# Kernel tuning notes

Hardware: AMD Instinct MI355X
Metric: run time of the kernel (lower is better)

The kernel has to match this reference:

```python
import jax, jax.numpy as jnp
import numpy as np

B, N_RELS, DICT, FEAT, LAT = 2048, 512, 2000, 300, 512
TOPK, DISK, T = 3, 20, 0.07


def setup_inputs() -> dict:
    key = jax.random.key(0)
    ks = jax.random.split(key, 24)
    p = lambda i, s: jax.random.normal(ks[i], s, jnp.float32) * 0.05
    return {
        "logits": jax.random.normal(ks[0], (B, N_RELS), jnp.float32),
        "rels": jax.random.randint(ks[1], (N_RELS, 2), 0, DICT, jnp.int32),
        "rel_dict": jax.random.uniform(ks[2], (DICT, FEAT), jnp.float32),
        "fc1_w": p(3, (2 * FEAT, 300)), "fc1_b": p(4, (300,)),
        "fc2mu_w": p(5, (300, LAT)), "fc2mu_b": p(6, (LAT,)),
        "fc2ls_w": p(7, (300, LAT)), "fc2ls_b": p(8, (LAT,)),
        "fc3_w": p(9, (LAT + FEAT, 300)), "fc3_b": p(10, (300,)),
        "fc4_w": p(11, (300, FEAT)), "fc4_b": p(12, (FEAT,)),
        "qi1_w": p(13, (FEAT, 512)), "qi1_b": p(14, (512,)),
        "qi2_w": p(15, (512, 512)), "qi2_b": p(16, (512,)),
        "qz1_w": p(17, (LAT, 512)), "qz1_b": p(18, (512,)),
        "qz2_w": p(19, (512, 512)), "qz2_b": p(20, (512,)),
        "eps1": jax.random.normal(ks[21], (B, LAT), jnp.float32),
        "eps2": jax.random.normal(ks[22], (B, LAT), jnp.float32),
    }


def _enc2(v, w1, b1, w2, b2):
    # two-layer MLP with LeakyReLU(0.2), matches nn.Sequential in MoCo
    h = jax.nn.leaky_relu(v @ w1 + b1, 0.2)
    return jax.nn.leaky_relu(h @ w2 + b2, 0.2)


def reference(logits, rels, rel_dict, fc1_w, fc1_b, fc2mu_w, fc2mu_b,
              fc2ls_w, fc2ls_b, fc3_w, fc3_b, fc4_w, fc4_b,
              qi1_w, qi1_b, qi2_w, qi2_b, qz1_w, qz1_b, qz2_w, qz2_b,
              eps1, eps2):
    # top-3 (descending sort head) and bottom-20 (ascending sort head)
    _, top_idx = jax.lax.top_k(logits, TOPK)            # [B,3]
    _, dis_idx = jax.lax.top_k(-logits, DISK)           # [B,20]
    pos = rel_dict[rels[top_idx, 1]]                    # [B,3,FEAT]
    pos1 = pos[:, 0]                                    # [B,FEAT] condition / MoCo positive
    x = pos[:, 0] * pos[:, 1] * pos[:, 2]               # elementwise product of top-3 dict vecs
    neg = rel_dict[rels[dis_idx, 1]]                    # [B,20,FEAT]

    # CVAE encode / reparametrize / decode (batched over the python loop)
    h1 = jax.nn.relu(jnp.concatenate([x, pos1], axis=-1) @ fc1_w + fc1_b)
    mu = h1 @ fc2mu_w + fc2mu_b                          # [B,512]
    log_std = h1 @ fc2ls_w + fc2ls_b                     # [B,512]
    std = jnp.exp(log_std)
    z = mu + eps1 * std
    h3 = jax.nn.relu(jnp.concatenate([z, pos1], axis=-1) @ fc3_w + fc3_b)
    recon = jax.nn.sigmoid(h3 @ fc4_w + fc4_b)           # [B,FEAT]
    recon_loss = jnp.sum((recon - x) ** 2)
    kl = jnp.sum(-0.5 * (1.0 + 2.0 * log_std - mu ** 2 - jnp.exp(2.0 * log_std)))
    loss_vae = (recon_loss + kl).reshape(1)

    # second reparametrize draw feeds MoCo
    z_ = mu + eps2 * std

    # MoCo: encoder_k == encoder_inp (copied at init; momentum update preserves equality)
    z_p = _enc2(z_, qz1_w, qz1_b, qz2_w, qz2_b)          # [B,512]
    pos_vec = _enc2(pos1, qi1_w, qi1_b, qi2_w, qi2_b)    # [B,512]
    neg_p = jax.lax.stop_gradient(_enc2(neg, qi1_w, qi1_b, qi2_w, qi2_b))  # [B,20,512]
    pos_l = jnp.sum(z_p * pos_vec, axis=-1, keepdims=True)                 # [B,1]
    neg_l = jnp.einsum('bd,bnd->bn', z_p, neg_p)                           # [B,20]
    lg = jnp.concatenate([pos_l, neg_l], axis=-1) / T                      # [B,21]
    # per-sample CE with label 0 (batch=1 in original loop), summed across loop
    loss_csl = jnp.sum(-jax.nn.log_softmax(lg, axis=-1)[:, 0]).reshape(1)

    z_rel = jnp.concatenate([jnp.zeros((1, z_p.shape[1]), z_p.dtype), z_p], axis=0)  # [B+1,512]
    return loss_vae, loss_csl, z_rel
```

## Files before the change

kernel.cpp:

```cpp
#include <hip/hip_runtime.h>
#include <math.h>

#define B      2048
#define NRELS  512
#define FEAT   300
#define LAT    512

typedef __attribute__((ext_vector_type(8))) short short8;
typedef __attribute__((ext_vector_type(4))) float f32x4;

__device__ inline short f2bf(float f) {
    union { float f; unsigned u; } v; v.f = f;
    unsigned u = v.u;
    u += 0x7fffu + ((u >> 16) & 1u);
    return (short)(u >> 16);
}

struct WDesc { const float* src; short* dst; int K, N, Kpad, Npad, ilv, ilvoff; };
struct WPack { WDesc d[9]; };

__global__ __launch_bounds__(256) void stage0(WPack p,
                                              const float* __restrict__ logits,
                                              const int* __restrict__ rels,
                                              const float* __restrict__ rel_dict,
                                              int* __restrict__ top_idx,
                                              int* __restrict__ dis_idx,
                                              short* __restrict__ xcat,
                                              float* __restrict__ xf,
                                              short* __restrict__ zcat,
                                              short* __restrict__ Rb,
                                              float* __restrict__ acc,
                                              float* __restrict__ out)
{
    const int bid = blockIdx.x;
    if (bid < 512) {
        if (bid == 0 && threadIdx.x >= 252) ((unsigned*)acc)[threadIdx.x - 252] = 0u;
        int lane = threadIdx.x & 63;
        int row  = bid * 4 + (threadIdx.x >> 6);
        const float* pl = logits + (size_t)row * NRELS;
        float v[8];
#pragma unroll
        for (int j = 0; j < 8; ++j) v[j] = pl[j * 64 + lane];
        float w[8];
#pragma unroll
        for (int j = 0; j < 8; ++j) w[j] = v[j];
        for (int t = 0; t < 20; ++t) {
            float bv = __builtin_inff(); int bi = 0x7fffffff;
#pragma unroll
            for (int j = 0; j < 8; ++j) {
                int idx = j * 64 + lane;
                if (w[j] < bv || (w[j] == bv && idx < bi)) { bv = w[j]; bi = idx; }
            }
#pragma unroll
            for (int off = 32; off >= 1; off >>= 1) {
                float ov = __shfl_xor(bv, off);
                int   oi = __shfl_xor(bi, off);
                if (ov < bv || (ov == bv && oi < bi)) { bv = ov; bi = oi; }
            }
            if ((bi & 63) == lane) w[bi >> 6] = __builtin_inff();
            if (lane == 0) dis_idx[row * 20 + t] = bi;
        }
        int t3[3];
#pragma unroll
        for (int j = 0; j < 8; ++j) w[j] = v[j];
        for (int t = 0; t < 3; ++t) {
            float bv = -__builtin_inff(); int bi = 0x7fffffff;
#pragma unroll
            for (int j = 0; j < 8; ++j) {
                int idx = j * 64 + lane;
                if (w[j] > bv || (w[j] == bv && idx < bi)) { bv = w[j]; bi = idx; }
            }
#pragma unroll
            for (int off = 32; off >= 1; off >>= 1) {
                float ov = __shfl_xor(bv, off);
                int   oi = __shfl_xor(bi, off);
                if (ov > bv || (ov == bv && oi < bi)) { bv = ov; bi = oi; }
            }
            if ((bi & 63) == lane) w[bi >> 6] = -__builtin_inff();
            t3[t] = bi;
        }
        if (lane == 0) top_idx[row] = t3[0];
        int i0 = rels[2 * t3[0] + 1];
        int i1 = rels[2 * t3[1] + 1];
        int i2 = rels[2 * t3[2] + 1];
        const float* r0 = rel_dict + (size_t)i0 * FEAT;
        const float* r1 = rel_dict + (size_t)i1 * FEAT;
        const float* r2 = rel_dict + (size_t)i2 * FEAT;
        short* xd  = xcat + (size_t)row * 640;
        short* zd  = zcat + (size_t)row * 832;
        float* xfd = xf   + (size_t)row * 300;
        for (int c = lane; c < FEAT; c += 64) {
            float a = r0[c];
            float x = a * r1[c] * r2[c];
            xd[c]       = f2bf(x);
            xd[300 + c] = f2bf(a);
            zd[512 + c] = f2bf(a);
            xfd[c]      = x;
        }
        if (lane < 40) xd[600 + lane] = 0;
        if (lane < 20) zd[812 + lane] = 0;
    } else if (bid < 640) {
        int lane = threadIdx.x & 63;
        int j = (bid - 512) * 4 + (threadIdx.x >> 6);
        int id = rels[2 * j + 1];
        const float* src = rel_dict + (size_t)id * FEAT;
        for (int c = lane; c < 320; c += 64)
            Rb[(size_t)j * 320 + c] = (c < FEAT) ? f2bf(src[c]) : (short)0;
    } else if (bid < 928) {
        int rel = bid - 640;
        WDesc w = p.d[rel >> 5];
        int b32 = rel & 31;
        if (!w.ilv) {
            int total = w.Npad * w.Kpad;
            for (int i = b32 * 256 + threadIdx.x; i < total; i += 32 * 256) {
                int n = i / w.Kpad, k = i - n * w.Kpad;
                w.dst[i] = (n < w.N && k < w.K) ? f2bf(w.src[(size_t)k * w.N + n]) : (short)0;
            }
        } else {
            int total = w.N * w.Kpad;
            for (int i = b32 * 256 + threadIdx.x; i < total; i += 32 * 256) {
                int c = i / w.Kpad, k = i - c * w.Kpad;
                int n = ((c >> 5) << 6) + w.ilvoff + (c & 31);
                w.dst[(size_t)n * w.Kpad + k] = (k < w.K) ? f2bf(w.src[(size_t)k * w.N + c]) : (short)0;
            }
        }
    } else {
        out[2 + threadIdx.x]       = 0.f;
        out[2 + 256 + threadIdx.x] = 0.f;
    }
}

template<int ACT, int MODE>
__device__ __attribute__((always_inline)) void gemm_core(
    short (&As)[64][72], short (&Bs)[64][72],
    int bx, int by,
    const short* __restrict__ A, const short* __restrict__ Bt,
    const float* __restrict__ bias, const float* __restrict__ bias2,
    void* __restrict__ Cv, int Nreal, int Kpad, int ldc,
    const float* __restrict__ aux0, const float* __restrict__ aux1,
    short* __restrict__ z0, short* __restrict__ z1,
    float* __restrict__ accv)
{
    const int wave = threadIdx.x >> 6;
    const int lane = threadIdx.x & 63;
    const int row0 = by * 64;
    const int col0 = bx * 64;

    const int srow = threadIdx.x >> 3;
    const int sk   = (threadIdx.x & 7) * 8;
    const short* Ap0 = A  + (size_t)(row0 + srow)      * Kpad + sk;
    const short* Ap1 = A  + (size_t)(row0 + srow + 32) * Kpad + sk;
    const short* Bp0 = Bt + (size_t)(col0 + srow)      * Kpad + sk;
    const short* Bp1 = Bt + (size_t)(col0 + srow + 32) * Kpad + sk;

    const int frow = lane & 15;
    const int fk   = (lane >> 4) * 8;

    f32x4 acc0 = {0,0,0,0}, acc1 = {0,0,0,0}, acc2 = {0,0,0,0}, acc3 = {0,0,0,0};

    short8 a0 = *(const short8*)Ap0;
    short8 a1 = *(const short8*)Ap1;
    short8 b0 = *(const short8*)Bp0;
    short8 b1 = *(const short8*)Bp1;

    for (int k0 = 0; k0 < Kpad; k0 += 64) {
        *(short8*)&As[srow][sk]      = a0;
        *(short8*)&As[srow + 32][sk] = a1;
        *(short8*)&Bs[srow][sk]      = b0;
        *(short8*)&Bs[srow + 32][sk] = b1;
        __syncthreads();
        int kn = k0 + 64;
        if (kn < Kpad) {
            a0 = *(const short8*)(Ap0 + kn);
            a1 = *(const short8*)(Ap1 + kn);
            b0 = *(const short8*)(Bp0 + kn);
            b1 = *(const short8*)(Bp1 + kn);
        }
        short8 af0 = *(const short8*)&As[wave * 16 + frow][fk];
        short8 af1 = *(const short8*)&As[wave * 16 + frow][fk + 32];
        short8 bf00 = *(const short8*)&Bs[ 0 + frow][fk];
        short8 bf01 = *(const short8*)&Bs[ 0 + frow][fk + 32];
        short8 bf10 = *(const short8*)&Bs[16 + frow][fk];
        short8 bf11 = *(const short8*)&Bs[16 + frow][fk + 32];
        short8 bf20 = *(const short8*)&Bs[32 + frow][fk];
        short8 bf21 = *(const short8*)&Bs[32 + frow][fk + 32];
        short8 bf30 = *(const short8*)&Bs[48 + frow][fk];
        short8 bf31 = *(const short8*)&Bs[48 + frow][fk + 32];
        acc0 = __builtin_amdgcn_mfma_f32_16x16x32_bf16(af0, bf00, acc0, 0, 0, 0);
        acc1 = __builtin_amdgcn_mfma_f32_16x16x32_bf16(af0, bf10, acc1, 0, 0, 0);
        acc2 = __builtin_amdgcn_mfma_f32_16x16x32_bf16(af0, bf20, acc2, 0, 0, 0);
        acc3 = __builtin_amdgcn_mfma_f32_16x16x32_bf16(af0, bf30, acc3, 0, 0, 0);
        acc0 = __builtin_amdgcn_mfma_f32_16x16x32_bf16(af1, bf01, acc0, 0, 0, 0);
        acc1 = __builtin_amdgcn_mfma_f32_16x16x32_bf16(af1, bf11, acc1, 0, 0, 0);
        acc2 = __builtin_amdgcn_mfma_f32_16x16x32_bf16(af1, bf21, acc2, 0, 0, 0);
        acc3 = __builtin_amdgcn_mfma_f32_16x16x32_bf16(af1, bf31, acc3, 0, 0, 0);
        __syncthreads();
    }

    const int orow = row0 + wave * 16 + (lane >> 4) * 4;
    f32x4 accs[4] = {acc0, acc1, acc2, acc3};

    if (MODE == 3) {
        float kls = 0.f;
#pragma unroll
        for (int n0 = 0; n0 < 2; ++n0) {
            int zc = bx * 32 + n0 * 16 + frow;
            float bmu = bias[zc];
            float bls = bias2[zc];
#pragma unroll
            for (int j = 0; j < 4; ++j) {
                int row = orow + j;
                float m = accs[n0][j]     + bmu;
                float l = accs[n0 + 2][j] + bls;
                float s = expf(l);
                size_t ei = (size_t)row * 512 + zc;
                z0[(size_t)row * 832 + zc] = f2bf(m + aux0[ei] * s);
                z1[ei]                     = f2bf(m + aux1[ei] * s);
                kls += -0.5f * (1.f + 2.f * l - m * m - expf(2.f * l));
            }
        }
#pragma unroll
        for (int off = 32; off >= 1; off >>= 1) kls += __shfl_xor(kls, off);
        __shared__ float redS[4];
        if (lane == 0) redS[wave] = kls;
        __syncthreads();
        if (threadIdx.x == 0) atomicAdd(accv, redS[0] + redS[1] + redS[2] + redS[3]);
        return;
    }

    float fsum = 0.f;
#pragma unroll
    for (int n0 = 0; n0 < 4; ++n0) {
        int col = col0 + n0 * 16 + frow;
        float bs = bias[col < Nreal ? col : Nreal - 1];
#pragma unroll
        for (int j = 0; j < 4; ++j) {
            float v = accs[n0][j] + bs;
            if (ACT == 1)      v = v > 0.f ? v : 0.f;
            else if (ACT == 2) v = v > 0.f ? v : 0.2f * v;
            else if (ACT == 3) v = 1.f / (1.f + expf(-v));
            if (MODE == 2) {
                if (col < Nreal) {
                    float d = v - aux0[(size_t)(orow + j) * 300 + col];
                    fsum += d * d;
                }
            } else {
                size_t idx = (size_t)(orow + j) * ldc + col;
                if (MODE == 1) ((float*)Cv)[idx] = v;
                else           ((short*)Cv)[idx] = f2bf(v);
            }
        }
    }
    if (MODE == 2) {
#pragma unroll
        for (int off = 32; off >= 1; off >>= 1) fsum += __shfl_xor(fsum, off);
        __shared__ float redF[4];
        if (lane == 0) redF[wave] = fsum;
        __syncthreads();
        if (threadIdx.x == 0) atomicAdd(accv, redF[0] + redF[1] + redF[2] + redF[3]);
    }
}

__global__ __launch_bounds__(256) void stage1(const short* Rb, const short* w_qi1t, const float* qi1_b, short* Ehb,
                                              const short* xcat, const short* w_fc1t, const float* fc1_b, short* h1)
{
    __shared__ short As[64][72];
    __shared__ short Bs[64][72];
    int b = blockIdx.x;
    if (b < 64)
        gemm_core<2,0>(As, Bs, b & 7, b >> 3, Rb, w_qi1t, qi1_b, qi1_b, Ehb, 512, 320, 512,
                       nullptr, nullptr, nullptr, nullptr, nullptr);
    else {
        b -= 64;
        gemm_core<1,0>(As, Bs, b % 5, b / 5, xcat, w_fc1t, fc1_b, fc1_b, h1, 300, 640, 320,
                       nullptr, nullptr, nullptr, nullptr, nullptr);
    }
}

__global__ __launch_bounds__(256) void stage2(const short* Ehb, const short* w_qi2t, const float* qi2_b, float* E,
                                              const short* h1, const short* w_mulst,
                                              const float* mu_b, const float* ls_b,
                                              const float* eps1, const float* eps2,
                                              short* zcat, short* zb, float* acc)
{
    __shared__ short As[64][72];
    __shared__ short Bs[64][72];
    int b = blockIdx.x;
    if (b < 64)
        gemm_core<2,1>(As, Bs, b & 7, b >> 3, Ehb, w_qi2t, qi2_b, qi2_b, E, 512, 512, 512,
                       nullptr, nullptr, nullptr, nullptr, nullptr);
    else {
        b -= 64;
        gemm_core<0,3>(As, Bs, b & 15, b >> 4, h1, w_mulst, mu_b, ls_b, nullptr, 1024, 320, 0,
                       eps1, eps2, zcat, zb, acc);
    }
}

__global__ __launch_bounds__(256) void stage3(const short* zcat, const short* w_fc3t, const float* fc3_b, short* h3,
                                              const short* zb, const short* w_qz1t, const float* qz1_b, short* t1)
{
    __shared__ short As[64][72];
    __shared__ short Bs[64][72];
    int b = blockIdx.x;
    if (b < 160)
        gemm_core<1,0>(As, Bs, b % 5, b / 5, zcat, w_fc3t, fc3_b, fc3_b, h3, 300, 832, 320,
                       nullptr, nullptr, nullptr, nullptr, nullptr);
    else {
        b -= 160;
        gemm_core<2,0>(As, Bs, b & 7, b >> 3, zb, w_qz1t, qz1_b, qz1_b, t1, 512, 512, 512,
                       nullptr, nullptr, nullptr, nullptr, nullptr);
    }
}

__global__ __launch_bounds__(256) void stage4(const short* h3, const short* w_fc4t, const float* fc4_b,
                                              const float* xf, float* acc,
                                              const short* t1, const short* w_qz2t, const float* qz2_b, float* zp)
{
    __shared__ short As[64][72];
    __shared__ short Bs[64][72];
    int b = blockIdx.x;
    if (b < 160)
        gemm_core<3,2>(As, Bs, b % 5, b / 5, h3, w_fc4t, fc4_b, fc4_b, nullptr, 300, 320, 0,
                       xf, nullptr, nullptr, nullptr, acc + 1);
    else {
        b -= 160;
        gemm_core<2,1>(As, Bs, b & 7, b >> 3, t1, w_qz2t, qz2_b, qz2_b, zp, 512, 512, 512,
                       nullptr, nullptr, nullptr, nullptr, nullptr);
    }
}

__global__ __launch_bounds__(256) void stage5(const float* __restrict__ zp,
                                              const float* __restrict__ E,
                                              const int* __restrict__ top_idx,
                                              const int* __restrict__ dis_idx,
                                              float* __restrict__ acc,
                                              float* __restrict__ out)
{
    int lane = threadIdx.x & 63;
    int wave = threadIdx.x >> 6;
    int r    = blockIdx.x * 4 + wave;
    const float* z = zp + (size_t)r * LAT;
    const float4 za = reinterpret_cast<const float4*>(z)[lane * 2 + 0];
    const float4 zb = reinterpret_cast<const float4*>(z)[lane * 2 + 1];

    int ids[21];
    ids[0] = top_idx[r];
#pragma unroll
    for (int n = 0; n < 20; ++n) ids[n + 1] = dis_idx[r * 20 + n];

    float lg[21];
#pragma unroll
    for (int t = 0; t < 21; ++t) {
        const float* e = E + (size_t)ids[t] * LAT;
        const float4 ea = reinterpret_cast<const float4*>(e)[lane * 2 + 0];
        const float4 eb = reinterpret_cast<const float4*>(e)[lane * 2 + 1];
        float d = za.x * ea.x + za.y * ea.y + za.z * ea.z + za.w * ea.w
                + zb.x * eb.x + zb.y * eb.y + zb.z * eb.z + zb.w * eb.w;
#pragma unroll
        for (int off = 32; off >= 1; off >>= 1) d += __shfl_xor(d, off);
        lg[t] = d / 0.07f;
    }
    float m = lg[0];
#pragma unroll
    for (int t = 1; t < 21; ++t) m = fmaxf(m, lg[t]);
    float s = 0.f;
#pragma unroll
    for (int t = 0; t < 21; ++t) s += expf(lg[t] - m);
    float loss = logf(s) + m - lg[0];

    __shared__ float red[4];
    if (lane == 0) red[wave] = loss;
    __syncthreads();
    if (threadIdx.x == 0) {
        atomicAdd(&acc[2], red[0] + red[1] + red[2] + red[3]);
        __threadfence();
        unsigned old = atomicAdd((unsigned*)acc + 3, 1u);
        if (old == (unsigned)(gridDim.x - 1)) {
            __threadfence();
            volatile float* va = acc;
            out[0] = va[0] + va[1];
            out[1] = va[2];
        }
    }
}

extern "C" void kernel_launch(void* const* d_in, const int* in_sizes, int n_in,
                              void* d_out, int out_size, void* d_ws, size_t ws_size,
                              hipStream_t stream)
{
    const float* logits   = (const float*)d_in[0];
    const int*   rels     = (const int*)  d_in[1];
    const float* rel_dict = (const float*)d_in[2];
    const float* fc1_w    = (const float*)d_in[3];
    const float* fc1_b    = (const float*)d_in[4];
    const float* fc2mu_w  = (const float*)d_in[5];
    const float* fc2mu_b  = (const float*)d_in[6];
    const float* fc2ls_w  = (const float*)d_in[7];
    const float* fc2ls_b  = (const float*)d_in[8];
    const float* fc3_w    = (const float*)d_in[9];
    const float* fc3_b    = (const float*)d_in[10];
    const float* fc4_w    = (const float*)d_in[11];
    const float* fc4_b    = (const float*)d_in[12];
    const float* qi1_w    = (const float*)d_in[13];
    const float* qi1_b    = (const float*)d_in[14];
    const float* qi2_w    = (const float*)d_in[15];
    const float* qi2_b    = (const float*)d_in[16];
    const float* qz1_w    = (const float*)d_in[17];
    const float* qz1_b    = (const float*)d_in[18];
    const float* qz2_w    = (const float*)d_in[19];
    const float* qz2_b    = (const float*)d_in[20];
    const float* eps1     = (const float*)d_in[21];
    const float* eps2     = (const float*)d_in[22];
    float* out = (float*)d_out;

    char* wsb = (char*)d_ws;
    size_t off = 0;
    auto alloc = [&](size_t bytes) -> void* {
        off = (off + 255) & ~(size_t)255;
        void* p = wsb + off;
        off += bytes;
        return p;
    };
    float* acc     = (float*)alloc(16);
    int*   top_idx = (int*)  alloc((size_t)B * 4);
    int*   dis_idx = (int*)  alloc((size_t)B * 20 * 4);
    short* Rb      = (short*)alloc((size_t)NRELS * 320 * 2);
    short* Ehb     = (short*)alloc((size_t)NRELS * 512 * 2);
    float* E       = (float*)alloc((size_t)NRELS * 512 * 4);
    short* xcat    = (short*)alloc((size_t)B * 640 * 2);
    float* xf      = (float*)alloc((size_t)B * 300 * 4);
    short* h1      = (short*)alloc((size_t)B * 320 * 2);
    short* zcat    = (short*)alloc((size_t)B * 832 * 2);
    short* zb      = (short*)alloc((size_t)B * 512 * 2);
    short* h3      = (short*)alloc((size_t)B * 320 * 2);
    short* t1      = (short*)alloc((size_t)B * 512 * 2);

    short* w_qi1t  = (short*)alloc((size_t)512 * 320 * 2);
    short* w_qi2t  = (short*)alloc((size_t)512 * 512 * 2);
    short* w_fc1t  = (short*)alloc((size_t)320 * 640 * 2);
    short* w_mulst = (short*)alloc((size_t)1024 * 320 * 2);
    short* w_fc3t  = (short*)alloc((size_t)320 * 832 * 2);
    short* w_fc4t  = (short*)alloc((size_t)320 * 320 * 2);
    short* w_qz1t  = (short*)alloc((size_t)512 * 512 * 2);
    short* w_qz2t  = (short*)alloc((size_t)512 * 512 * 2);

    WPack p;
    p.d[0] = {qi1_w,   w_qi1t,  300, 512, 320,  512, 0, 0};
    p.d[1] = {qi2_w,   w_qi2t,  512, 512, 512,  512, 0, 0};
    p.d[2] = {fc1_w,   w_fc1t,  600, 300, 640,  320, 0, 0};
    p.d[3] = {fc2mu_w, w_mulst, 300, 512, 320, 1024, 1, 0};
    p.d[4] = {fc2ls_w, w_mulst, 300, 512, 320, 1024, 1, 32};
    p.d[5] = {fc3_w,   w_fc3t,  812, 300, 832,  320, 0, 0};
    p.d[6] = {fc4_w,   w_fc4t,  300, 300, 320,  320, 0, 0};
    p.d[7] = {qz1_w,   w_qz1t,  512, 512, 512,  512, 0, 0};
    p.d[8] = {qz2_w,   w_qz2t,  512, 512, 512,  512, 0, 0};

    float* zp = out + 2 + 512;

    stage0<<<929, 256, 0, stream>>>(p, logits, rels, rel_dict, top_idx, dis_idx,
                                    xcat, xf, zcat, Rb, acc, out);
    stage1<<<224, 256, 0, stream>>>(Rb, w_qi1t, qi1_b, Ehb, xcat, w_fc1t, fc1_b, h1);
    stage2<<<576, 256, 0, stream>>>(Ehb, w_qi2t, qi2_b, E, h1, w_mulst, fc2mu_b, fc2ls_b,
                                    eps1, eps2, zcat, zb, acc);
    stage3<<<416, 256, 0, stream>>>(zcat, w_fc3t, fc3_b, h3, zb, w_qz1t, qz1_b, t1);
    stage4<<<416, 256, 0, stream>>>(h3, w_fc4t, fc4_b, xf, acc, t1, w_qz2t, qz2_b, zp);
    stage5<<<B / 4, 256, 0, stream>>>(zp, E, top_idx, dis_idx, acc, out);
}
```

Before: 97.75 us.

## Use 128x64 GEMM tiles for batch GEMMs and tile-transpose weight conversion

Adds a gemm_tile path where each wave computes a 32x64 sub-tile, so each block covers 128 rows instead of 64 for the batch-sized GEMMs. This halves block counts and doubles reuse of the B tile per LDS load. The weight transpose-to-bf16 pass now stages 64x64 tiles through shared memory, giving coalesced reads and writes instead of strided global reads. The cost is fewer blocks per stage, which lowers occupancy and parallelism on a large GPU, plus a larger LDS footprint.

```diff
diff --git a/kernel.cpp b/kernel.cpp
--- a/kernel.cpp
+++ b/kernel.cpp
@@ -16,7 +16,7 @@
     return (short)(u >> 16);
 }
 
-struct WDesc { const float* src; short* dst; int K, N, Kpad, Npad, ilv, ilvoff; };
+struct WDesc { const float* src; short* dst; int K, N, Kpad, Npad, ilv, ilvoff, tstart, tk; };
 struct WPack { WDesc d[9]; };
 
 __global__ __launch_bounds__(256) void stage0(WPack p,
@@ -32,6 +32,7 @@
                                               float* __restrict__ acc,
                                               float* __restrict__ out)
 {
+    __shared__ float T[64][65];
     const int bid = blockIdx.x;
     if (bid < 512) {
         if (bid == 0 && threadIdx.x >= 252) ((unsigned*)acc)[threadIdx.x - 252] = 0u;
@@ -106,22 +107,40 @@
         const float* src = rel_dict + (size_t)id * FEAT;
         for (int c = lane; c < 320; c += 64)
             Rb[(size_t)j * 320 + c] = (c < FEAT) ? f2bf(src[c]) : (short)0;
-    } else if (bid < 928) {
-        int rel = bid - 640;
-        WDesc w = p.d[rel >> 5];
-        int b32 = rel & 31;
-        if (!w.ilv) {
-            int total = w.Npad * w.Kpad;
-            for (int i = b32 * 256 + threadIdx.x; i < total; i += 32 * 256) {
-                int n = i / w.Kpad, k = i - n * w.Kpad;
-                w.dst[i] = (n < w.N && k < w.K) ? f2bf(w.src[(size_t)k * w.N + n]) : (short)0;
-            }
-        } else {
-            int total = w.N * w.Kpad;
-            for (int i = b32 * 256 + threadIdx.x; i < total; i += 32 * 256) {
-                int c = i / w.Kpad, k = i - c * w.Kpad;
-                int n = ((c >> 5) << 6) + w.ilvoff + (c & 31);
-                w.dst[(size_t)n * w.Kpad + k] = (k < w.K) ? f2bf(w.src[(size_t)k * w.N + c]) : (short)0;
+    } else if (bid < 1092) {
+        int u = bid - 640;
+        int di = 0;
+#pragma unroll
+        for (int q = 1; q < 9; ++q) if (u >= p.d[q].tstart) di = q;
+        WDesc w = p.d[di];
+        int r  = u - w.tstart;
+        int kt = r % w.tk;
+        int nt = r / w.tk;
+        int k0 = kt * 64, n0 = nt * 64;
+
+        {
+            int kk = threadIdx.x >> 2;
+            int c0 = (threadIdx.x & 3) * 16;
+            int gk = k0 + kk;
+            const float* srow = w.src + (size_t)gk * w.N;
+            bool kin = gk < w.K;
+#pragma unroll
+            for (int j = 0; j < 16; ++j) {
+                int gn = n0 + c0 + j;
+                T[kk][c0 + j] = (kin && gn < w.N) ? srow[gn] : 0.f;
+            }
+        }
+        __syncthreads();
+        {
+            int nn = threadIdx.x >> 2;
+            int c0 = (threadIdx.x & 3) * 16;
+            int ns = n0 + nn;
+            if (ns < w.Npad || w.ilv) {
+                int nd = w.ilv ? (((ns >> 5) << 6) + w.ilvoff + (ns & 31)) : ns;
+                short* drow = w.dst + (size_t)nd * w.Kpad + k0;
+#pragma unroll
+                for (int j = 0; j < 16; ++j)
+                    drow[c0 + j] = f2bf(T[c0 + j][nn]);
             }
         }
     } else {
@@ -132,8 +151,85 @@
 
 template<int ACT, int MODE>
 __device__ __attribute__((always_inline)) void gemm_core(
-    short (&As)[64][72], short (&Bs)[64][72],
+    short (&As)[128][72], short (&Bs)[64][72],
     int bx, int by,
+    const short* __restrict__ A, const short* __restrict__ Bt,
+    const float* __restrict__ bias,
+    void* __restrict__ Cv, int Nreal, int Kpad, int ldc)
+{
+    const int wave = threadIdx.x >> 6;
+    const int lane = threadIdx.x & 63;
+    const int row0 = by * 64;
+    const int col0 = bx * 64;
+
+    const int srow = threadIdx.x >> 3;
+    const int sk   = (threadIdx.x & 7) * 8;
+    const short* Ap0 = A  + (size_t)(row0 + srow)      * Kpad + sk;
+    const short* Ap1 = A  + (size_t)(row0 + srow + 32) * Kpad + sk;
+    const short* Bp0 = Bt + (size_t)(col0 + srow)      * Kpad + sk;
+    const short* Bp1 = Bt + (size_t)(col0 + srow + 32) * Kpad + sk;
+
+    const int frow = lane & 15;
+    const int fk   = (lane >> 4) * 8;
+
+    f32x4 acc0 = {0,0,0,0}, acc1 = {0,0,0,0}, acc2 = {0,0,0,0}, acc3 = {0,0,0,0};
+
+    short8 a0 = *(const short8*)Ap0;
+    short8 a1 = *(const short8*)Ap1;
+    short8 b0 = *(const short8*)Bp0;
+    short8 b1 = *(const short8*)Bp1;
+
+    for (int k0 = 0; k0 < Kpad; k0 += 64) {
+        *(short8*)&As[srow][sk]      = a0;
+        *(short8*)&As[srow + 32][sk] = a1;
+        *(short8*)&Bs[srow][sk]      = b0;
+        *(short8*)&Bs[srow + 32][sk] = b1;
+        __syncthreads();
+        int kn = k0 + 64;
+        if (kn < Kpad) {
+            a0 = *(const short8*)(Ap0 + kn);
+            a1 = *(const short8*)(Ap1 + kn);
+            b0 = *(const short8*)(Bp0 + kn);
+            b1 = *(const short8*)(Bp1 + kn);
+        }
+#pragma unroll
+        for (int kk = 0; kk < 2; ++kk) {
+            short8 af = *(const short8*)&As[wave * 16 + frow][fk + kk * 32];
+            short8 bf0 = *(const short8*)&Bs[ 0 + frow][fk + kk * 32];
+            short8 bf1 = *(const short8*)&Bs[16 + frow][fk + kk * 32];
+            short8 bf2 = *(const short8*)&Bs[32 + frow][fk + kk * 32];
+            short8 bf3 = *(const short8*)&Bs[48 + frow][fk + kk * 32];
+            acc0 = __builtin_amdgcn_mfma_f32_16x16x32_bf16(af, bf0, acc0, 0, 0, 0);
+            acc1 = __builtin_amdgcn_mfma_f32_16x16x32_bf16(af, bf1, acc1, 0, 0, 0);
+            acc2 = __builtin_amdgcn_mfma_f32_16x16x32_bf16(af, bf2, acc2, 0, 0, 0);
+            acc3 = __builtin_amdgcn_mfma_f32_16x16x32_bf16(af, bf3, acc3, 0, 0, 0);
+        }
+        __syncthreads();
+    }
+
+    const int orow = row0 + wave * 16 + (lane >> 4) * 4;
+    f32x4 accs[4] = {acc0, acc1, acc2, acc3};
+#pragma unroll
+    for (int n0 = 0; n0 < 4; ++n0) {
+        int col = col0 + n0 * 16 + frow;
+        float bs = bias[col < Nreal ? col : Nreal - 1];
+#pragma unroll
+        for (int j = 0; j < 4; ++j) {
+            float v = accs[n0][j] + bs;
+            if (ACT == 1)      v = v > 0.f ? v : 0.f;
+            else if (ACT == 2) v = v > 0.f ? v : 0.2f * v;
+            else if (ACT == 3) v = 1.f / (1.f + expf(-v));
+            size_t idx = (size_t)(orow + j) * ldc + col;
+            if (MODE == 1) ((float*)Cv)[idx] = v;
+            else           ((short*)Cv)[idx] = f2bf(v);
+        }
+    }
+}
+
+template<int ACT, int MODE>
+__device__ __attribute__((always_inline)) void gemm_tile(
+    short (&As)[128][72], short (&Bs)[64][72],
+    int tx, int ty,
     const short* __restrict__ A, const short* __restrict__ Bt,
     const float* __restrict__ bias, const float* __restrict__ bias2,
     void* __restrict__ Cv, int Nreal, int Kpad, int ldc,
@@ -141,88 +237,91 @@
     short* __restrict__ z0, short* __restrict__ z1,
     float* __restrict__ accv)
 {
-    const int wave = threadIdx.x >> 6;
+    const int w    = threadIdx.x >> 6;
     const int lane = threadIdx.x & 63;
-    const int row0 = by * 64;
-    const int col0 = bx * 64;
-
-    const int srow = threadIdx.x >> 3;
-    const int sk   = (threadIdx.x & 7) * 8;
-    const short* Ap0 = A  + (size_t)(row0 + srow)      * Kpad + sk;
-    const short* Ap1 = A  + (size_t)(row0 + srow + 32) * Kpad + sk;
-    const short* Bp0 = Bt + (size_t)(col0 + srow)      * Kpad + sk;
-    const short* Bp1 = Bt + (size_t)(col0 + srow + 32) * Kpad + sk;
-
+    const int row0 = ty * 128, col0 = tx * 64;
+
+    const int sr = threadIdx.x >> 3;
+    const int sk = (threadIdx.x & 7) * 8;
+    const short* Ap = A  + (size_t)(row0 + sr) * Kpad + sk;
+    const short* Bp = Bt + (size_t)(col0 + sr) * Kpad + sk;
     const int frow = lane & 15;
     const int fk   = (lane >> 4) * 8;
 
-    f32x4 acc0 = {0,0,0,0}, acc1 = {0,0,0,0}, acc2 = {0,0,0,0}, acc3 = {0,0,0,0};
-
-    short8 a0 = *(const short8*)Ap0;
-    short8 a1 = *(const short8*)Ap1;
-    short8 b0 = *(const short8*)Bp0;
-    short8 b1 = *(const short8*)Bp1;
+    f32x4 acc[2][4] = {};
+
+    short8 ra0 = *(const short8*)(Ap);
+    short8 ra1 = *(const short8*)(Ap + (size_t)32 * Kpad);
+    short8 ra2 = *(const short8*)(Ap + (size_t)64 * Kpad);
+    short8 ra3 = *(const short8*)(Ap + (size_t)96 * Kpad);
+    short8 rb0 = *(const short8*)(Bp);
+    short8 rb1 = *(const short8*)(Bp + (size_t)32 * Kpad);
 
     for (int k0 = 0; k0 < Kpad; k0 += 64) {
-        *(short8*)&As[srow][sk]      = a0;
-        *(short8*)&As[srow + 32][sk] = a1;
-        *(short8*)&Bs[srow][sk]      = b0;
-        *(short8*)&Bs[srow + 32][sk] = b1;
+        *(short8*)&As[sr     ][sk] = ra0;
+        *(short8*)&As[sr + 32][sk] = ra1;
+        *(short8*)&As[sr + 64][sk] = ra2;
+        *(short8*)&As[sr + 96][sk] = ra3;
+        *(short8*)&Bs[sr     ][sk] = rb0;
+        *(short8*)&Bs[sr + 32][sk] = rb1;
         __syncthreads();
         int kn = k0 + 64;
         if (kn < Kpad) {
-            a0 = *(const short8*)(Ap0 + kn);
-            a1 = *(const short8*)(Ap1 + kn);
-            b0 = *(const short8*)(Bp0 + kn);
-            b1 = *(const short8*)(Bp1 + kn);
-        }
-        short8 af0 = *(const short8*)&As[wave * 16 + frow][fk];
-        short8 af1 = *(const short8*)&As[wave * 16 + frow][fk + 32];
-        short8 bf00 = *(const short8*)&Bs[ 0 + frow][fk];
-        short8 bf01 = *(const short8*)&Bs[ 0 + frow][fk + 32];
-        short8 bf10 = *(const short8*)&Bs[16 + frow][fk];
-        short8 bf11 = *(const short8*)&Bs[16 + frow][fk + 32];
-        short8 bf20 = *(const short8*)&Bs[32 + frow][fk];
-        short8 bf21 = *(const short8*)&Bs[32 + frow][fk + 32];
-        short8 bf30 = *(const short8*)&Bs[48 + frow][fk];
-        short8 bf31 = *(const short8*)&Bs[48 + frow][fk + 32];
-        acc0 = __builtin_amdgcn_mfma_f32_16x16x32_bf16(af0, bf00, acc0, 0, 0, 0);
-        acc1 = __builtin_amdgcn_mfma_f32_16x16x32_bf16(af0, bf10, acc1, 0, 0, 0);
-        acc2 = __builtin_amdgcn_mfma_f32_16x16x32_bf16(af0, bf20, acc2, 0, 0, 0);
-        acc3 = __builtin_amdgcn_mfma_f32_16x16x32_bf16(af0, bf30, acc3, 0, 0, 0);
-        acc0 = __builtin_amdgcn_mfma_f32_16x16x32_bf16(af1, bf01, acc0, 0, 0, 0);
-        acc1 = __builtin_amdgcn_mfma_f32_16x16x32_bf16(af1, bf11, acc1, 0, 0, 0);
-        acc2 = __builtin_amdgcn_mfma_f32_16x16x32_bf16(af1, bf21, acc2, 0, 0, 0);
-        acc3 = __builtin_amdgcn_mfma_f32_16x16x32_bf16(af1, bf31, acc3, 0, 0, 0);
-        __syncthreads();
-    }
-
-    const int orow = row0 + wave * 16 + (lane >> 4) * 4;
-    f32x4 accs[4] = {acc0, acc1, acc2, acc3};
+            ra0 = *(const short8*)(Ap + kn);
+            ra1 = *(const short8*)(Ap + (size_t)32 * Kpad + kn);
+            ra2 = *(const short8*)(Ap + (size_t)64 * Kpad + kn);
+            ra3 = *(const short8*)(Ap + (size_t)96 * Kpad + kn);
+            rb0 = *(const short8*)(Bp + kn);
+            rb1 = *(const short8*)(Bp + (size_t)32 * Kpad + kn);
+        }
+#pragma unroll
+        for (int kk = 0; kk < 2; ++kk) {
+            short8 a0 = *(const short8*)&As[w * 32 +      frow][fk + kk * 32];
+            short8 a1 = *(const short8*)&As[w * 32 + 16 + frow][fk + kk * 32];
+            short8 b0 = *(const short8*)&Bs[ 0 + frow][fk + kk * 32];
+            short8 b1 = *(const short8*)&Bs[16 + frow][fk + kk * 32];
+            short8 b2 = *(const short8*)&Bs[32 + frow][fk + kk * 32];
+            short8 b3 = *(const short8*)&Bs[48 + frow][fk + kk * 32];
+            acc[0][0] = __builtin_amdgcn_mfma_f32_16x16x32_bf16(a0, b0, acc[0][0], 0, 0, 0);
+            acc[0][1] = __builtin_amdgcn_mfma_f32_16x16x32_bf16(a0, b1, acc[0][1], 0, 0, 0);
+            acc[0][2] = __builtin_amdgcn_mfma_f32_16x16x32_bf16(a0, b2, acc[0][2], 0, 0, 0);
+            acc[0][3] = __builtin_amdgcn_mfma_f32_16x16x32_bf16(a0, b3, acc[0][3], 0, 0, 0);
+            acc[1][0] = __builtin_amdgcn_mfma_f32_16x16x32_bf16(a1, b0, acc[1][0], 0, 0, 0);
+            acc[1][1] = __builtin_amdgcn_mfma_f32_16x16x32_bf16(a1, b1, acc[1][1], 0, 0, 0);
+            acc[1][2] = __builtin_amdgcn_mfma_f32_16x16x32_bf16(a1, b2, acc[1][2], 0, 0, 0);
+            acc[1][3] = __builtin_amdgcn_mfma_f32_16x16x32_bf16(a1, b3, acc[1][3], 0, 0, 0);
+        }
+        __syncthreads();
+    }
+
+    const int rbase = row0 + w * 32 + (lane >> 4) * 4;
 
     if (MODE == 3) {
         float kls = 0.f;
 #pragma unroll
-        for (int n0 = 0; n0 < 2; ++n0) {
-            int zc = bx * 32 + n0 * 16 + frow;
-            float bmu = bias[zc];
-            float bls = bias2[zc];
-#pragma unroll
-            for (int j = 0; j < 4; ++j) {
-                int row = orow + j;
-                float m = accs[n0][j]     + bmu;
-                float l = accs[n0 + 2][j] + bls;
-                float s = expf(l);
-                size_t ei = (size_t)row * 512 + zc;
-                z0[(size_t)row * 832 + zc] = f2bf(m + aux0[ei] * s);
-                z1[ei]                     = f2bf(m + aux1[ei] * s);
-                kls += -0.5f * (1.f + 2.f * l - m * m - expf(2.f * l));
+        for (int mr = 0; mr < 2; ++mr) {
+#pragma unroll
+            for (int nc = 0; nc < 2; ++nc) {
+                int zc = tx * 32 + nc * 16 + frow;
+                float bmu = bias[zc];
+                float bls = bias2[zc];
+#pragma unroll
+                for (int j = 0; j < 4; ++j) {
+                    int row = rbase + mr * 16 + j;
+                    float m = acc[mr][nc][j]     + bmu;
+                    float l = acc[mr][nc + 2][j] + bls;
+                    float s = expf(l);
+                    size_t ei = (size_t)row * 512 + zc;
+                    z0[(size_t)row * 832 + zc] = f2bf(m + aux0[ei] * s);
+                    z1[ei]                     = f2bf(m + aux1[ei] * s);
+                    kls += -0.5f * (1.f + 2.f * l - m * m - expf(2.f * l));
+                }
             }
         }
 #pragma unroll
         for (int off = 32; off >= 1; off >>= 1) kls += __shfl_xor(kls, off);
         __shared__ float redS[4];
-        if (lane == 0) redS[wave] = kls;
+        if (lane == 0) redS[w] = kls;
         __syncthreads();
         if (threadIdx.x == 0) atomicAdd(accv, redS[0] + redS[1] + redS[2] + redS[3]);
         return;
@@ -230,24 +329,28 @@
 
     float fsum = 0.f;
 #pragma unroll
-    for (int n0 = 0; n0 < 4; ++n0) {
-        int col = col0 + n0 * 16 + frow;
-        float bs = bias[col < Nreal ? col : Nreal - 1];
-#pragma unroll
-        for (int j = 0; j < 4; ++j) {
-            float v = accs[n0][j] + bs;
-            if (ACT == 1)      v = v > 0.f ? v : 0.f;
-            else if (ACT == 2) v = v > 0.f ? v : 0.2f * v;
-            else if (ACT == 3) v = 1.f / (1.f + expf(-v));
-            if (MODE == 2) {
-                if (col < Nreal) {
-                    float d = v - aux0[(size_t)(orow + j) * 300 + col];
-                    fsum += d * d;
+    for (int mr = 0; mr < 2; ++mr) {
+#pragma unroll
+        for (int nc = 0; nc < 4; ++nc) {
+            int col = col0 + nc * 16 + frow;
+            float bs = bias[col < Nreal ? col : Nreal - 1];
+#pragma unroll
+            for (int j = 0; j < 4; ++j) {
+                float v = acc[mr][nc][j] + bs;
+                if (ACT == 1)      v = v > 0.f ? v : 0.f;
+                else if (ACT == 2) v = v > 0.f ? v : 0.2f * v;
+                else if (ACT == 3) v = 1.f / (1.f + expf(-v));
+                int row = rbase + mr * 16 + j;
+                if (MODE == 2) {
+                    if (col < Nreal) {
+                        float d = v - aux0[(size_t)row * 300 + col];
+                        fsum += d * d;
+                    }
+                } else {
+                    size_t idx = (size_t)row * ldc + col;
+                    if (MODE == 1) ((float*)Cv)[idx] = v;
+                    else           ((short*)Cv)[idx] = f2bf(v);
                 }
-            } else {
-                size_t idx = (size_t)(orow + j) * ldc + col;
-                if (MODE == 1) ((float*)Cv)[idx] = v;
-                else           ((short*)Cv)[idx] = f2bf(v);
             }
         }
     }
@@ -255,7 +358,7 @@
 #pragma unroll
         for (int off = 32; off >= 1; off >>= 1) fsum += __shfl_xor(fsum, off);
         __shared__ float redF[4];
-        if (lane == 0) redF[wave] = fsum;
+        if (lane == 0) redF[w] = fsum;
         __syncthreads();
         if (threadIdx.x == 0) atomicAdd(accv, redF[0] + redF[1] + redF[2] + redF[3]);
     }
@@ -264,16 +367,15 @@
 __global__ __launch_bounds__(256) void stage1(const short* Rb, const short* w_qi1t, const float* qi1_b, short* Ehb,
                                               const short* xcat, const short* w_fc1t, const float* fc1_b, short* h1)
 {
-    __shared__ short As[64][72];
+    __shared__ short As[128][72];
     __shared__ short Bs[64][72];
     int b = blockIdx.x;
     if (b < 64)
-        gemm_core<2,0>(As, Bs, b & 7, b >> 3, Rb, w_qi1t, qi1_b, qi1_b, Ehb, 512, 320, 512,
-                       nullptr, nullptr, nullptr, nullptr, nullptr);
+        gemm_core<2,0>(As, Bs, b & 7, b >> 3, Rb, w_qi1t, qi1_b, Ehb, 512, 320, 512);
     else {
         b -= 64;
-        gemm_core<1,0>(As, Bs, b % 5, b / 5, xcat, w_fc1t, fc1_b, fc1_b, h1, 300, 640, 320,
-                       nullptr, nullptr, nullptr, nullptr, nullptr);
+        gemm_tile<1,0>(As, Bs, b % 5, b / 5, xcat, w_fc1t, fc1_b, nullptr,
+                       h1, 300, 640, 320, nullptr, nullptr, nullptr, nullptr, nullptr);
     }
 }
 
@@ -283,32 +385,31 @@
                                               const float* eps1, const float* eps2,
                                               short* zcat, short* zb, float* acc)
 {
-    __shared__ short As[64][72];
+    __shared__ short As[128][72];
     __shared__ short Bs[64][72];
     int b = blockIdx.x;
     if (b < 64)
-        gemm_core<2,1>(As, Bs, b & 7, b >> 3, Ehb, w_qi2t, qi2_b, qi2_b, E, 512, 512, 512,
-                       nullptr, nullptr, nullptr, nullptr, nullptr);
+        gemm_core<2,1>(As, Bs, b & 7, b >> 3, Ehb, w_qi2t, qi2_b, E, 512, 512, 512);
     else {
         b -= 64;
-        gemm_core<0,3>(As, Bs, b & 15, b >> 4, h1, w_mulst, mu_b, ls_b, nullptr, 1024, 320, 0,
-                       eps1, eps2, zcat, zb, acc);
+        gemm_tile<0,3>(As, Bs, b & 15, b >> 4, h1, w_mulst, mu_b, ls_b,
+                       nullptr, 1024, 320, 0, eps1, eps2, zcat, zb, acc + 0);
     }
 }
 
 __global__ __launch_bounds__(256) void stage3(const short* zcat, const short* w_fc3t, const float* fc3_b, short* h3,
                                               const short* zb, const short* w_qz1t, const float* qz1_b, short* t1)
 {
-    __shared__ short As[64][72];
+    __shared__ short As[128][72];
     __shared__ short Bs[64][72];
     int b = blockIdx.x;
-    if (b < 160)
-        gemm_core<1,0>(As, Bs, b % 5, b / 5, zcat, w_fc3t, fc3_b, fc3_b, h3, 300, 832, 320,
-                       nullptr, nullptr, nullptr, nullptr, nullptr);
+    if (b < 80)
+        gemm_tile<1,0>(As, Bs, b % 5, b / 5, zcat, w_fc3t, fc3_b, nullptr,
+                       h3, 300, 832, 320, nullptr, nullptr, nullptr, nullptr, nullptr);
     else {
-        b -= 160;
-        gemm_core<2,0>(As, Bs, b & 7, b >> 3, zb, w_qz1t, qz1_b, qz1_b, t1, 512, 512, 512,
-                       nullptr, nullptr, nullptr, nullptr, nullptr);
+        b -= 80;
+        gemm_tile<2,0>(As, Bs, b & 7, b >> 3, zb, w_qz1t, qz1_b, nullptr,
+                       t1, 512, 512, 512, nullptr, nullptr, nullptr, nullptr, nullptr);
     }
 }
 
@@ -316,16 +417,16 @@
                                               const float* xf, float* acc,
                                               const short* t1, const short* w_qz2t, const float* qz2_b, float* zp)
 {
-    __shared__ short As[64][72];
+    __shared__ short As[128][72];
     __shared__ short Bs[64][72];
     int b = blockIdx.x;
-    if (b < 160)
-        gemm_core<3,2>(As, Bs, b % 5, b / 5, h3, w_fc4t, fc4_b, fc4_b, nullptr, 300, 320, 0,
-                       xf, nullptr, nullptr, nullptr, acc + 1);
+    if (b < 80)
+        gemm_tile<3,2>(As, Bs, b % 5, b / 5, h3, w_fc4t, fc4_b, nullptr,
+                       nullptr, 300, 320, 0, xf, nullptr, nullptr, nullptr, acc + 1);
     else {
-        b -= 160;
-        gemm_core<2,1>(As, Bs, b & 7, b >> 3, t1, w_qz2t, qz2_b, qz2_b, zp, 512, 512, 512,
-                       nullptr, nullptr, nullptr, nullptr, nullptr);
+        b -= 80;
+        gemm_tile<2,1>(As, Bs, b & 7, b >> 3, t1, w_qz2t, qz2_b, nullptr,
+                       zp, 512, 512, 512, nullptr, nullptr, nullptr, nullptr, nullptr);
     }
 }
 
@@ -445,24 +546,24 @@
     short* w_qz2t  = (short*)alloc((size_t)512 * 512 * 2);
 
     WPack p;
-    p.d[0] = {qi1_w,   w_qi1t,  300, 512, 320,  512, 0, 0};
-    p.d[1] = {qi2_w,   w_qi2t,  512, 512, 512,  512, 0, 0};
-    p.d[2] = {fc1_w,   w_fc1t,  600, 300, 640,  320, 0, 0};
-    p.d[3] = {fc2mu_w, w_mulst, 300, 512, 320, 1024, 1, 0};
-    p.d[4] = {fc2ls_w, w_mulst, 300, 512, 320, 1024, 1, 32};
-    p.d[5] = {fc3_w,   w_fc3t,  812, 300, 832,  320, 0, 0};
-    p.d[6] = {fc4_w,   w_fc4t,  300, 300, 320,  320, 0, 0};
-    p.d[7] = {qz1_w,   w_qz1t,  512, 512, 512,  512, 0, 0};
-    p.d[8] = {qz2_w,   w_qz2t,  512, 512, 512,  512, 0, 0};
+    p.d[0] = {qi1_w,   w_qi1t,  300, 512, 320,  512, 0, 0,    0,  5};
+    p.d[1] = {qi2_w,   w_qi2t,  512, 512, 512,  512, 0, 0,   40,  8};
+    p.d[2] = {fc1_w,   w_fc1t,  600, 300, 640,  320, 0, 0,  104, 10};
+    p.d[3] = {fc2mu_w, w_mulst, 300, 512, 320, 1024, 1, 0,  154,  5};
+    p.d[4] = {fc2ls_w, w_mulst, 300, 512, 320, 1024, 1, 32, 194,  5};
+    p.d[5] = {fc3_w,   w_fc3t,  812, 300, 832,  320, 0, 0,  234, 13};
+    p.d[6] = {fc4_w,   w_fc4t,  300, 300, 320,  320, 0, 0,  299,  5};
+    p.d[7] = {qz1_w,   w_qz1t,  512, 512, 512,  512, 0, 0,  324,  8};
+    p.d[8] = {qz2_w,   w_qz2t,  512, 512, 512,  512, 0, 0,  388,  8};
 
     float* zp = out + 2 + 512;
 
-    stage0<<<929, 256, 0, stream>>>(p, logits, rels, rel_dict, top_idx, dis_idx,
-                                    xcat, xf, zcat, Rb, acc, out);
-    stage1<<<224, 256, 0, stream>>>(Rb, w_qi1t, qi1_b, Ehb, xcat, w_fc1t, fc1_b, h1);
-    stage2<<<576, 256, 0, stream>>>(Ehb, w_qi2t, qi2_b, E, h1, w_mulst, fc2mu_b, fc2ls_b,
+    stage0<<<1093, 256, 0, stream>>>(p, logits, rels, rel_dict, top_idx, dis_idx,
+                                     xcat, xf, zcat, Rb, acc, out);
+    stage1<<<144, 256, 0, stream>>>(Rb, w_qi1t, qi1_b, Ehb, xcat, w_fc1t, fc1_b, h1);
+    stage2<<<320, 256, 0, stream>>>(Ehb, w_qi2t, qi2_b, E, h1, w_mulst, fc2mu_b, fc2ls_b,
                                     eps1, eps2, zcat, zb, acc);
-    stage3<<<416, 256, 0, stream>>>(zcat, w_fc3t, fc3_b, h3, zb, w_qz1t, qz1_b, t1);
-    stage4<<<416, 256, 0, stream>>>(h3, w_fc4t, fc4_b, xf, acc, t1, w_qz2t, qz2_b, zp);
+    stage3<<<208, 256, 0, stream>>>(zcat, w_fc3t, fc3_b, h3, zb, w_qz1t, qz1_b, t1);
+    stage4<<<208, 256, 0, stream>>>(h3, w_fc4t, fc4_b, xf, acc, t1, w_qz2t, qz2_b, zp);
     stage5<<<B / 4, 256, 0, stream>>>(zp, E, top_idx, dis_idx, acc, out);
 }
```

Result: slower. 104.3 us (+6.7%).
